# Kernel optimization log

Measured on AMD Instinct MI355X. Metric: run time of the kernel, lower is better.

## Reference

```python
import jax, jax.numpy as jnp
import numpy as np

RES = 16; NC = 256; NCP = 1024; KNN = 32; SIGMA = 0.1
DM = 256; NH = 8; FF = 1024; NLAYERS = 2
E = NC * 8 * (RES // 8) ** 2
EH = 8
B = 4; N = 65536


def setup_inputs() -> dict:
    key = jax.random.key(0)
    ks = jax.random.split(key, 16)
    s = 0.02
    def w(k, shape):
        return jax.random.normal(k, shape, jnp.float32) * s
    inp = {}
    inp['pc'] = jax.random.normal(ks[0], (B, N, 3), jnp.float32)
    inp['pe_w1'] = w(ks[1], (3, 128)); inp['pe_b1'] = jnp.zeros((128,), jnp.float32)
    inp['pe_w2'] = w(ks[2], (128, 128)); inp['pe_b2'] = jnp.zeros((128,), jnp.float32)
    inp['t_qkv_w'] = w(ks[3], (NLAYERS, DM, 3 * DM)); inp['t_qkv_b'] = jnp.zeros((NLAYERS, 3 * DM), jnp.float32)
    inp['t_out_w'] = w(ks[4], (NLAYERS, DM, DM)); inp['t_out_b'] = jnp.zeros((NLAYERS, DM), jnp.float32)
    inp['t_ln1_s'] = jnp.ones((NLAYERS, DM), jnp.float32); inp['t_ln1_b'] = jnp.zeros((NLAYERS, DM), jnp.float32)
    inp['t_ff1_w'] = w(ks[5], (NLAYERS, DM, FF)); inp['t_ff1_b'] = jnp.zeros((NLAYERS, FF), jnp.float32)
    inp['t_ff2_w'] = w(ks[6], (NLAYERS, FF, DM)); inp['t_ff2_b'] = jnp.zeros((NLAYERS, DM), jnp.float32)
    inp['t_ln2_s'] = jnp.ones((NLAYERS, DM), jnp.float32); inp['t_ln2_b'] = jnp.zeros((NLAYERS, DM), jnp.float32)
    inp['c1_w'] = w(ks[7], (2 * NC, NC, 3, 3)); inp['c1_b'] = jnp.zeros((2 * NC,), jnp.float32)
    inp['c2_w'] = w(ks[8], (4 * NC, 2 * NC, 3, 3)); inp['c2_b'] = jnp.zeros((4 * NC,), jnp.float32)
    inp['c3_w'] = w(ks[9], (8 * NC, 4 * NC, 3, 3)); inp['c3_b'] = jnp.zeros((8 * NC,), jnp.float32)
    inp['x_qkv_w'] = w(ks[10], (E, 3 * E)); inp['x_qkv_b'] = jnp.zeros((3 * E,), jnp.float32)
    inp['x_out_w'] = w(ks[11], (E, E)); inp['x_out_b'] = jnp.zeros((E,), jnp.float32)
    return inp


def _layernorm(x, s, b):
    m = x.mean(-1, keepdims=True)
    v = ((x - m) ** 2).mean(-1, keepdims=True)
    return (x - m) / jnp.sqrt(v + 1e-5) * s + b


def _mha(x, qkv_w, qkv_b, out_w, out_b, nh):
    Bq, S, D = x.shape
    dh = D // nh
    qkv = x @ qkv_w + qkv_b
    q, k, v = jnp.split(qkv, 3, axis=-1)
    def sp(t):
        return t.reshape(Bq, S, nh, dh).transpose(0, 2, 1, 3)
    q, k, v = sp(q), sp(k), sp(v)
    a = jax.nn.softmax(jnp.einsum('bhqd,bhkd->bhqk', q, k) / jnp.sqrt(jnp.float32(dh)), axis=-1)
    o = jnp.einsum('bhqk,bhkd->bhqd', a, v).transpose(0, 2, 1, 3).reshape(Bq, S, D)
    return o @ out_w + out_b


def _density(pc):
    # faithful to source: distance to the FIRST k points (unsorted), not kNN
    d = jnp.linalg.norm(pc[:, :, None, :] - pc[:, None, :KNN, :], axis=-1)  # (B,N,k)
    return jnp.exp(-2.0 * SIGMA ** 2 / (d * d + 1e-6)).mean(axis=-1)


def _fps_indices(pc, density):
    # incremental min-dist FPS: selects identical points to the original O(N*K^2) loop
    def one(pc_b, dens_b):
        first = jnp.argmax(dens_b)
        mind = jnp.linalg.norm(pc_b - pc_b[first], axis=-1)
        def step(mind, _):
            idx = jnp.argmax(mind)
            d = jnp.linalg.norm(pc_b - pc_b[idx], axis=-1)
            return jnp.minimum(mind, d), idx
        _, rest = jax.lax.scan(step, mind, None, length=NCP - 1)
        return jnp.concatenate([first[None], rest])
    return jax.vmap(one)(pc, density)


def _forward(pc, idx, pe_w1, pe_b1, pe_w2, pe_b2, t_qkv_w, t_qkv_b, t_out_w, t_out_b,
             t_ln1_s, t_ln1_b, t_ff1_w, t_ff1_b, t_ff2_w, t_ff2_b, t_ln2_s, t_ln2_b,
             c1_w, c1_b, c2_w, c2_b, c3_w, c3_b, x_qkv_w, x_qkv_b, x_out_w, x_out_b):
    Bq = pc.shape[0]
    centers = jnp.take_along_axis(pc, idx[:, :, None], axis=1)  # (B,K,3)
    # point encoder MLP -> (B,K,128)
    f = jax.nn.relu(centers @ pe_w1 + pe_b1) @ pe_w2 + pe_b2
    # sinusoidal pos-emb per axis, mean over xyz -> (B,K,128)
    half = 64
    freqs = jnp.exp(jnp.arange(half, dtype=jnp.float32) * (-np.log(10000.0) / (half - 1)))
    e = centers[..., None] * freqs  # (B,K,3,64)
    pos = jnp.concatenate([jnp.sin(e), jnp.cos(e)], axis=-1).mean(axis=2)
    x = jnp.concatenate([f, pos], axis=-1)  # (B,K,256)
    # 2-layer post-LN transformer encoder
    for l in range(NLAYERS):
        h = _mha(x, t_qkv_w[l], t_qkv_b[l], t_out_w[l], t_out_b[l], NH)
        x = _layernorm(x + h, t_ln1_s[l], t_ln1_b[l])
        h = jax.nn.relu(x @ t_ff1_w[l] + t_ff1_b[l]) @ t_ff2_w[l] + t_ff2_b[l]
        x = _layernorm(x + h, t_ln2_s[l], t_ln2_b[l])
    # scatter-add features onto three planes
    L = pc.max() - pc.min()
    def grid(c):
        return jnp.clip(((c + L / 2) / L * RES).astype(jnp.int32), 0, RES - 1)
    gx = grid(centers[..., 0]); gy = grid(centers[..., 1]); gz = grid(centers[..., 2])
    tri = jnp.zeros((Bq, 3, RES, RES, DM), jnp.float32)  # channels last for scatter
    bi = jnp.arange(Bq)[:, None]
    tri = tri.at[bi, 0, gy, gx].add(x)
    tri = tri.at[bi, 1, gz, gy].add(x)
    tri = tri.at[bi, 2, gz, gx].add(x)
    tri = tri.transpose(0, 1, 4, 2, 3)  # (B,3,C,R,R)
    z = tri.reshape(Bq * 3, DM, RES, RES)
    def conv(xx, w, b):
        y = jax.lax.conv_general_dilated(xx, w, (2, 2), ((1, 1), (1, 1)),
                                         dimension_numbers=('NCHW', 'OIHW', 'NCHW'))
        return y + b[None, :, None, None]
    z = jax.nn.relu(conv(z, c1_w, c1_b))
    z = jax.nn.relu(conv(z, c2_w, c2_b))
    z = jax.nn.relu(conv(z, c3_w, c3_b))  # (B*3, 8C, R/8, R/8)
    flat = z.reshape(Bq, 3, E)
    attn = _mha(flat, x_qkv_w, x_qkv_b, x_out_w, x_out_b, EH)
    return attn.reshape(Bq, 3, 8 * NC, RES // 8, RES // 8)


def reference(pc, pe_w1, pe_b1, pe_w2, pe_b2, t_qkv_w, t_qkv_b, t_out_w, t_out_b,
              t_ln1_s, t_ln1_b, t_ff1_w, t_ff1_b, t_ff2_w, t_ff2_b, t_ln2_s, t_ln2_b,
              c1_w, c1_b, c2_w, c2_b, c3_w, c3_b, x_qkv_w, x_qkv_b, x_out_w, x_out_b):
    idx = _fps_indices(pc, _density(pc))
    return _forward(pc, idx, pe_w1, pe_b1, pe_w2, pe_b2, t_qkv_w, t_qkv_b, t_out_w, t_out_b,
                    t_ln1_s, t_ln1_b, t_ff1_w, t_ff1_b, t_ff2_w, t_ff2_b, t_ln2_s, t_ln2_b,
                    c1_w, c1_b, c2_w, c2_b, c3_w, c3_b, x_qkv_w, x_qkv_b, x_out_w, x_out_b)
```

## Files before the change

### kernel.cpp

```cpp
#include <hip/hip_runtime.h>
#include <math.h>

#define NPTS   65536
#define NBATCH 4
#define KCP    1024
#define DM     256
#define FFD    1024
#define EDIM   8192
#define N3E    24576

#define FPS_NBLK 16
#define FPS_THR  256
#define FPS_PPT  16
#define GPUB     8
#define HARV_MAX 16
#define RING     16

__device__ __forceinline__ unsigned long long umaxll(unsigned long long a, unsigned long long b) {
  return a > b ? a : b;
}

__global__ __launch_bounds__(256) void redmm_kernel(const float* __restrict__ v, int n,
                                                    float* __restrict__ pmax, float* __restrict__ pmin) {
  float mx = -INFINITY, mn = INFINITY;
  for (int i = blockIdx.x * 256 + threadIdx.x; i < n; i += gridDim.x * 256) {
    float x = v[i]; mx = fmaxf(mx, x); mn = fminf(mn, x);
  }
#pragma unroll
  for (int off = 32; off >= 1; off >>= 1) {
    mx = fmaxf(mx, __shfl_xor(mx, off, 64));
    mn = fminf(mn, __shfl_xor(mn, off, 64));
  }
  __shared__ float smx[4], smn[4];
  int lane = threadIdx.x & 63, w = threadIdx.x >> 6;
  if (lane == 0) { smx[w] = mx; smn[w] = mn; }
  __syncthreads();
  if (threadIdx.x == 0) {
    pmax[blockIdx.x] = fmaxf(fmaxf(smx[0], smx[1]), fmaxf(smx[2], smx[3]));
    pmin[blockIdx.x] = fminf(fminf(smn[0], smn[1]), fminf(smn[2], smn[3]));
  }
}

__global__ __launch_bounds__(256) void redfin_kernel(const float* __restrict__ pmax,
                                                     const float* __restrict__ pmin, int nb,
                                                     float* __restrict__ Lv) {
  float mx = -INFINITY, mn = INFINITY;
  for (int i = threadIdx.x; i < nb; i += 256) { mx = fmaxf(mx, pmax[i]); mn = fminf(mn, pmin[i]); }
#pragma unroll
  for (int off = 32; off >= 1; off >>= 1) {
    mx = fmaxf(mx, __shfl_xor(mx, off, 64));
    mn = fminf(mn, __shfl_xor(mn, off, 64));
  }
  __shared__ float smx[4], smn[4];
  int lane = threadIdx.x & 63, w = threadIdx.x >> 6;
  if (lane == 0) { smx[w] = mx; smn[w] = mn; }
  __syncthreads();
  if (threadIdx.x == 0) {
    mx = fmaxf(fmaxf(smx[0], smx[1]), fmaxf(smx[2], smx[3]));
    mn = fminf(fminf(smn[0], smn[1]), fminf(smn[2], smn[3]));
    Lv[0] = __fsub_rn(mx, mn);
  }
}

__global__ __launch_bounds__(FPS_THR, 1) void fps_kernel(const float* __restrict__ pc,
                                                         float* __restrict__ centers,
                                                         unsigned* __restrict__ tags,
                                                         unsigned long long* __restrict__ keys) {
  const int blk = blockIdx.x;
  const int b = blk / FPS_NBLK, bb = blk % FPS_NBLK;
  const int tid = threadIdx.x;
  const int lane = tid & 63, wv = tid >> 6;
  const int wvg = bb * 4 + wv;
  const float* pcb = pc + (size_t)b * NPTS * 3;

  __shared__ float kpts[96];

  float px[FPS_PPT], py[FPS_PPT], pz[FPS_PPT], mind[FPS_PPT];
  const int gbase = wvg * 1024;
#pragma unroll
  for (int i = 0; i < FPS_PPT; ++i) {
    int g = gbase + i * 64 + lane;
    px[i] = pcb[3 * g]; py[i] = pcb[3 * g + 1]; pz[i] = pcb[3 * g + 2];
  }
  for (int i = tid; i < 96; i += FPS_THR) kpts[i] = pcb[i];
  __syncthreads();

  unsigned* const tagb = tags + (size_t)b * RING * 64;
  unsigned long long* const keyb = keys + (size_t)b * RING * 512;

  auto exchange = [&](const unsigned long long* ek, int nk, int r,
                      unsigned long long* ck) {
    const int ri = r & (RING - 1);
    if (lane == 0) {
      unsigned long long* sp = keyb + (size_t)ri * 512 + wvg * 8;
      for (int g = 0; g < nk; ++g)
        __hip_atomic_store(&sp[g], ek[g], __ATOMIC_RELAXED, __HIP_MEMORY_SCOPE_AGENT);
      __hip_atomic_store(&tagb[ri * 64 + wvg], (unsigned)r, __ATOMIC_RELEASE, __HIP_MEMORY_SCOPE_AGENT);
    }
    unsigned tag;
    do {
      tag = __hip_atomic_load(&tagb[ri * 64 + lane], __ATOMIC_ACQUIRE, __HIP_MEMORY_SCOPE_AGENT);
    } while (__any(tag != (unsigned)r));
    const unsigned long long* pl = keyb + (size_t)ri * 512 + lane * 8;
    for (int e = 0; e < nk; ++e)
      ck[e] = __hip_atomic_load(&pl[e], __ATOMIC_RELAXED, __HIP_MEMORY_SCOPE_AGENT);
  };

  {
    unsigned long long bk = 0ull;
#pragma unroll
    for (int i = 0; i < FPS_PPT; ++i) {
      float acc = 0.f;
      for (int j = 0; j < 32; ++j) {
        float dx = __fsub_rn(px[i], kpts[3 * j]);
        float dy = __fsub_rn(py[i], kpts[3 * j + 1]);
        float dz = __fsub_rn(pz[i], kpts[3 * j + 2]);
        float ss = __fadd_rn(__fadd_rn(__fmul_rn(dx, dx), __fmul_rn(dy, dy)), __fmul_rn(dz, dz));
        float d = __fsqrt_rn(ss);
        float dd = __fadd_rn(__fmul_rn(d, d), 1e-6f);
        acc = __fadd_rn(acc, expf(__fdiv_rn(-0.02f, dd)));
      }
      float dens = __fdiv_rn(acc, 32.f);
      int g = gbase + i * 64 + lane;
      bk = umaxll(bk, ((unsigned long long)__float_as_uint(dens) << 32) | (unsigned int)(~g));
    }
#pragma unroll
    for (int off = 1; off < 64; off <<= 1) bk = umaxll(bk, __shfl_xor(bk, off, 64));
    unsigned long long ek[1] = { bk }, ck[1];
    exchange(ek, 1, 1, ck);
    unsigned long long k2 = ck[0];
#pragma unroll
    for (int off = 1; off < 64; off <<= 1) k2 = umaxll(k2, __shfl_xor(k2, off, 64));
    int widx = (int)(~(unsigned)(k2 & 0xFFFFFFFFull));
    float wx = pcb[3 * widx], wy = pcb[3 * widx + 1], wz = pcb[3 * widx + 2];
    if (wvg == 0 && lane == 0) {
      centers[(size_t)b * KCP * 3 + 0] = wx;
      centers[(size_t)b * KCP * 3 + 1] = wy;
      centers[(size_t)b * KCP * 3 + 2] = wz;
    }
#pragma unroll
    for (int i = 0; i < FPS_PPT; ++i) {
      float dx = __fsub_rn(px[i], wx), dy = __fsub_rn(py[i], wy), dz = __fsub_rn(pz[i], wz);
      mind[i] = __fsqrt_rn(__fadd_rn(__fadd_rn(__fmul_rn(dx, dx), __fmul_rn(dy, dy)), __fmul_rn(dz, dz)));
    }
  }

  int t = 1;
  for (int r = 2; t < KCP; ++r) {
    unsigned long long tk[FPS_PPT];
#pragma unroll
    for (int i = 0; i < FPS_PPT; ++i) {
      int g = gbase + i * 64 + lane;
      tk[i] = ((unsigned long long)__float_as_uint(mind[i]) << 32) | (unsigned int)(~g);
    }
    unsigned long long ek[GPUB];
#pragma unroll
    for (int g = 0; g < GPUB; ++g) {
      unsigned long long lbk = 0ull;
#pragma unroll
      for (int i = 0; i < FPS_PPT; ++i) lbk = umaxll(lbk, tk[i]);
      unsigned long long wk = lbk;
#pragma unroll
      for (int off = 1; off < 64; off <<= 1) wk = umaxll(wk, __shfl_xor(wk, off, 64));
      ek[g] = wk;
#pragma unroll
      for (int i = 0; i < FPS_PPT; ++i)
        if (tk[i] == wk) tk[i] = 0ull;
    }
    unsigned long long ck[GPUB];
    exchange(ek, GPUB, r, ck);
    float cx[GPUB], cy[GPUB], cz[GPUB];
#pragma unroll
    for (int e = 0; e < GPUB; ++e) {
      int gi = (int)(~(unsigned)(ck[e] & 0xFFFFFFFFull));
      cx[e] = pcb[3 * gi]; cy[e] = pcb[3 * gi + 1]; cz[e] = pcb[3 * gi + 2];
    }
    unsigned long long u = ck[GPUB - 1];
#pragma unroll
    for (int off = 1; off < 64; off <<= 1) u = umaxll(u, __shfl_xor(u, off, 64));
    int h = 0;
    while (true) {
      unsigned long long lb = 0ull; float lx = 0.f, ly = 0.f, lz = 0.f;
#pragma unroll
      for (int e = 0; e < GPUB; ++e)
        if (ck[e] > lb) { lb = ck[e]; lx = cx[e]; ly = cy[e]; lz = cz[e]; }
      unsigned long long wk = lb;
#pragma unroll
      for (int off = 1; off < 64; off <<= 1) wk = umaxll(wk, __shfl_xor(wk, off, 64));
      if (h > 0 && wk < u) break;
      int owner = __ffsll(__ballot(lb == wk)) - 1;
      float wx = __shfl(lx, owner, 64), wy = __shfl(ly, owner, 64), wz = __shfl(lz, owner, 64);
      if (wvg == 0 && lane == 0) {
        centers[((size_t)b * KCP + t) * 3 + 0] = wx;
        centers[((size_t)b * KCP + t) * 3 + 1] = wy;
        centers[((size_t)b * KCP + t) * 3 + 2] = wz;
      }
#pragma unroll
      for (int e = 0; e < GPUB; ++e) {
        float dx = __fsub_rn(cx[e], wx), dy = __fsub_rn(cy[e], wy), dz = __fsub_rn(cz[e], wz);
        float d = __fsqrt_rn(__fadd_rn(__fadd_rn(__fmul_rn(dx, dx), __fmul_rn(dy, dy)), __fmul_rn(dz, dz)));
        float ov = __uint_as_float((unsigned)(ck[e] >> 32));
        float nv = fminf(ov, d);
        ck[e] = ((unsigned long long)__float_as_uint(nv) << 32) | (ck[e] & 0xFFFFFFFFull);
      }
#pragma unroll
      for (int i = 0; i < FPS_PPT; ++i) {
        float dx = __fsub_rn(px[i], wx), dy = __fsub_rn(py[i], wy), dz = __fsub_rn(pz[i], wz);
        float d = __fsqrt_rn(__fadd_rn(__fadd_rn(__fmul_rn(dx, dx), __fmul_rn(dy, dy)), __fmul_rn(dz, dz)));
        mind[i] = fminf(mind[i], d);
      }
      ++h; ++t;
      if (h == HARV_MAX || t == KCP) break;
    }
  }
}

__global__ __launch_bounds__(128) void pe_kernel(const float* __restrict__ centers,
                                                 const float* __restrict__ w1, const float* __restrict__ b1,
                                                 const float* __restrict__ w2, const float* __restrict__ b2,
                                                 float* __restrict__ x) {
  const int p = blockIdx.x;
  const int d = threadIdx.x;
  __shared__ float h[128];
  __shared__ float c[3];
  if (d < 3) c[d] = centers[(size_t)p * 3 + d];
  __syncthreads();
  float hv = b1[d];
#pragma unroll
  for (int j = 0; j < 3; ++j) hv += c[j] * w1[j * 128 + d];
  hv = fmaxf(hv, 0.f);
  h[d] = hv;
  __syncthreads();
  float f = b2[d];
  for (int j = 0; j < 128; ++j) f += h[j] * w2[j * 128 + d];
  x[(size_t)p * 256 + d] = f;
  if (d < 64) {
    float fr = expf(__fmul_rn((float)d, -0.14619587892025696f));
    float ssum = 0.f, csum = 0.f;
#pragma unroll
    for (int a = 0; a < 3; ++a) {
      float e = __fmul_rn(c[a], fr);
      ssum += sinf(e); csum += cosf(e);
    }
    x[(size_t)p * 256 + 128 + d] = __fdiv_rn(ssum, 3.f);
    x[(size_t)p * 256 + 192 + d] = __fdiv_rn(csum, 3.f);
  }
}

__global__ __launch_bounds__(256) void gemm_kernel(const float* __restrict__ A, const float* __restrict__ W,
                                                   const float* __restrict__ bias, float* __restrict__ C,
                                                   int M, int Kd, int Nd, int relu) {
  __shared__ float As[16][65];
  __shared__ float Ws[16][65];
  const int bm = blockIdx.y * 64, bn = blockIdx.x * 64;
  const int tid = threadIdx.x;
  const int tx = tid & 15, ty = tid >> 4;
  float acc[4][4] = {};
  for (int k0 = 0; k0 < Kd; k0 += 16) {
#pragma unroll
    for (int i = 0; i < 4; ++i) {
      int f = tid + 256 * i; int k = f & 15, m = f >> 4;
      As[k][m] = A[(size_t)(bm + m) * Kd + k0 + k];
    }
#pragma unroll
    for (int i = 0; i < 4; ++i) {
      int f = tid + 256 * i; int n = f & 63, k = f >> 6;
      Ws[k][n] = W[(size_t)(k0 + k) * Nd + bn + n];
    }
    __syncthreads();
#pragma unroll
    for (int k = 0; k < 16; ++k) {
      float a[4], w[4];
#pragma unroll
      for (int i = 0; i < 4; ++i) a[i] = As[k][ty * 4 + i];
#pragma unroll
      for (int j = 0; j < 4; ++j) w[j] = Ws[k][tx * 4 + j];
#pragma unroll
      for (int i = 0; i < 4; ++i)
#pragma unroll
        for (int j = 0; j < 4; ++j) acc[i][j] += a[i] * w[j];
    }
    __syncthreads();
  }
#pragma unroll
  for (int i = 0; i < 4; ++i)
#pragma unroll
    for (int j = 0; j < 4; ++j) {
      float v = acc[i][j] + bias[bn + tx * 4 + j];
      if (relu) v = fmaxf(v, 0.f);
      C[(size_t)(bm + ty * 4 + i) * Nd + bn + tx * 4 + j] = v;
    }
}

__global__ __launch_bounds__(256, 1) void flash_kernel(const float* __restrict__ qkv, float* __restrict__ ao) {
  const int qt = blockIdx.x, h = blockIdx.y, b = blockIdx.z;
  const int tid = threadIdx.x;
  const int qi = tid >> 2, p = tid & 3;
  const int q0 = qt * 64;
  __shared__ float Kc[64][36];
  __shared__ float Vc[64][36];
  __shared__ float Sc[64][68];

  float4 q4[8];
  const float* qrow = qkv + (size_t)(b * 1024 + q0 + qi) * 768 + h * 32;
#pragma unroll
  for (int i = 0; i < 8; ++i) q4[i] = ((const float4*)qrow)[i];

  float o0[4] = {0, 0, 0, 0}, o1[4] = {0, 0, 0, 0};
  float m_cur = -INFINITY, l_part = 0.f;
  const int d0 = p * 8;

  for (int c0 = 0; c0 < 1024; c0 += 64) {
    for (int i = tid; i < 64 * 32; i += 256) {
      int j = i >> 5, d = i & 31;
      size_t row = (size_t)(b * 1024 + c0 + j) * 768;
      Kc[j][d] = qkv[row + 256 + h * 32 + d];
      Vc[j][d] = qkv[row + 512 + h * 32 + d];
    }
    __syncthreads();
    float sreg[16];
#pragma unroll 4
    for (int jj = 0; jj < 16; ++jj) {
      int j = p + 4 * jj;
      const float* kr = &Kc[j][0];
      float s = 0.f;
#pragma unroll
      for (int i = 0; i < 8; ++i) {
        float4 kv = *(const float4*)(kr + 4 * i);
        s += q4[i].x * kv.x + q4[i].y * kv.y + q4[i].z * kv.z + q4[i].w * kv.w;
      }
      sreg[jj] = s * 0.17677669529663687f;
    }
    float cmax = sreg[0];
#pragma unroll
    for (int jj = 1; jj < 16; ++jj) cmax = fmaxf(cmax, sreg[jj]);
    cmax = fmaxf(cmax, __shfl_xor(cmax, 1, 64));
    cmax = fmaxf(cmax, __shfl_xor(cmax, 2, 64));
    float m_new = fmaxf(m_cur, cmax);
    float corr = expf(m_cur - m_new);
    l_part *= corr;
#pragma unroll
    for (int i = 0; i < 4; ++i) { o0[i] *= corr; o1[i] *= corr; }
#pragma unroll
    for (int jj = 0; jj < 16; ++jj) {
      float pv = expf(sreg[jj] - m_new);
      l_part += pv;
      Sc[qi][p + 4 * jj] = pv;
    }
    m_cur = m_new;
    for (int j = 0; j < 64; ++j) {
      float pj = Sc[qi][j];
      float4 va = *(const float4*)(&Vc[j][d0]);
      float4 vb = *(const float4*)(&Vc[j][d0 + 4]);
      o0[0] += pj * va.x; o0[1] += pj * va.y; o0[2] += pj * va.z; o0[3] += pj * va.w;
      o1[0] += pj * vb.x; o1[1] += pj * vb.y; o1[2] += pj * vb.z; o1[3] += pj * vb.w;
    }
    __syncthreads();
  }
  float l2 = l_part + __shfl_xor(l_part, 1, 64);
  float lt = l2 + __shfl_xor(l2, 2, 64);
  float inv = 1.f / lt;
  float* orow = ao + (size_t)(b * 1024 + q0 + qi) * 256 + h * 32 + d0;
#pragma unroll
  for (int i = 0; i < 4; ++i) orow[i] = o0[i] * inv;
#pragma unroll
  for (int i = 0; i < 4; ++i) orow[4 + i] = o1[i] * inv;
}

__global__ __launch_bounds__(256) void ln_kernel(const float* __restrict__ a, const float* __restrict__ r,
                                                 const float* __restrict__ sc, const float* __restrict__ bi,
                                                 float* __restrict__ out) {
  const int row = blockIdx.x * 4 + (threadIdx.x >> 6);
  const int lane = threadIdx.x & 63;
  const float* ar = a + (size_t)row * 256;
  const float* rr = r + (size_t)row * 256;
  float v[4];
#pragma unroll
  for (int i = 0; i < 4; ++i) v[i] = ar[lane + 64 * i] + rr[lane + 64 * i];
  float s = v[0] + v[1] + v[2] + v[3];
#pragma unroll
  for (int off = 32; off >= 1; off >>= 1) s += __shfl_xor(s, off, 64);
  float mean = s * (1.f / 256.f);
  float vs = 0.f;
#pragma unroll
  for (int i = 0; i < 4; ++i) { float d = v[i] - mean; vs += d * d; }
#pragma unroll
  for (int off = 32; off >= 1; off >>= 1) vs += __shfl_xor(vs, off, 64);
  float var = vs * (1.f / 256.f);
  float rstd = 1.f / sqrtf(var + 1e-5f);
  float* orow = out + (size_t)row * 256;
#pragma unroll
  for (int i = 0; i < 4; ++i) {
    int d = lane + 64 * i;
    orow[d] = (v[i] - mean) * rstd * sc[d] + bi[d];
  }
}

__global__ __launch_bounds__(256) void scatter_kernel(const float* __restrict__ x,
                                                      const float* __restrict__ centers,
                                                      const float* __restrict__ Lv,
                                                      float* __restrict__ tri) {
  const int pnt = blockIdx.x;
  const int b = pnt >> 10;
  const int tid = threadIdx.x;
  __shared__ int g[3];
  if (tid == 0) {
    float L = Lv[0];
    float half = __fmul_rn(L, 0.5f);
#pragma unroll
    for (int a = 0; a < 3; ++a) {
      float c = centers[(size_t)pnt * 3 + a];
      float t = __fmul_rn(__fdiv_rn(__fadd_rn(c, half), L), 16.f);
      int gi = (int)t;
      g[a] = min(15, max(0, gi));
    }
  }
  __syncthreads();
  const int gx = g[0], gy = g[1], gz = g[2];
  float v = x[(size_t)pnt * 256 + tid];
  float* trib = tri + (size_t)b * 3 * 256 * 256;
  atomicAdd(&trib[(0 * 256 + tid) * 256 + gy * 16 + gx], v);
  atomicAdd(&trib[(1 * 256 + tid) * 256 + gz * 16 + gy], v);
  atomicAdd(&trib[(2 * 256 + tid) * 256 + gz * 16 + gx], v);
}

template <int IC, int OC, int IH, int IW, int OH, int OW, int OCT, int ICC>
__global__ __launch_bounds__(256, 1) void conv_kernel(const float* __restrict__ in, const float* __restrict__ w,
                                                      const float* __restrict__ bias, float* __restrict__ out) {
  __shared__ float lin[ICC * IH * IW];
  const int n = blockIdx.x;
  const int oc = blockIdx.y * OCT + threadIdx.x / (OH * OW);
  const int sp = threadIdx.x % (OH * OW);
  const int oy = sp / OW, ox = sp % OW;
  const int iy0 = oy * 2 - 1, ix0 = ox * 2 - 1;
  float acc = 0.f;
  for (int c0 = 0; c0 < IC; c0 += ICC) {
    __syncthreads();
    for (int i = threadIdx.x; i < ICC * IH * IW; i += 256)
      lin[i] = in[((size_t)n * IC + c0) * (IH * IW) + i];
    __syncthreads();
    const float* wp = w + ((size_t)oc * IC + c0) * 9;
    for (int ic = 0; ic < ICC; ++ic) {
      const float* wr = wp + (size_t)ic * 9;
      const float* lr = lin + ic * IH * IW;
#pragma unroll
      for (int ky = 0; ky < 3; ++ky) {
        int iy = iy0 + ky;
        if (iy >= 0 && iy < IH) {
#pragma unroll
          for (int kx = 0; kx < 3; ++kx) {
            int ix = ix0 + kx;
            if (ix >= 0 && ix < IW) acc += lr[iy * IW + ix] * wr[ky * 3 + kx];
          }
        }
      }
    }
  }
  out[((size_t)n * OC + oc) * (OH * OW) + sp] = fmaxf(acc + bias[oc], 0.f);
}

__global__ void biasinit_kernel(float* __restrict__ out, const float* __restrict__ bias, int M, int N) {
  int i = blockIdx.x * 256 + threadIdx.x;
  if (i < M * N) out[i] = bias[i % N];
}

template <int M, int KC>
__global__ __launch_bounds__(256, 1) void matvec_kernel(const float* __restrict__ A, const float* __restrict__ W,
                                                        float* __restrict__ out, int Kd, int Nd) {
  __shared__ float Al[KC * M];
  const int tid = threadIdx.x;
  const int n = blockIdx.x * 256 + tid;
  const int k0 = blockIdx.y * KC;
  for (int i = tid; i < KC * M; i += 256) {
    int k = i / M, m = i - k * M;
    Al[i] = A[(size_t)m * Kd + k0 + k];
  }
  __syncthreads();
  float acc[M] = {};
  for (int k = 0; k < KC; ++k) {
    float wv = W[(size_t)(k0 + k) * Nd + n];
#pragma unroll
    for (int m = 0; m < M; ++m) acc[m] += Al[k * M + m] * wv;
  }
#pragma unroll
  for (int m = 0; m < M; ++m) atomicAdd(&out[(size_t)m * Nd + n], acc[m]);
}

__global__ __launch_bounds__(256) void attn3_kernel(const float* __restrict__ qkv, float* __restrict__ o) {
  const int b = blockIdx.x >> 3, h = blockIdx.x & 7;
  const float* base = qkv + (size_t)b * 3 * N3E;
  const int qo = h * 1024, ko = EDIM + h * 1024, vo = 2 * EDIM + h * 1024;
  float p[9] = {};
  for (int d = threadIdx.x; d < 1024; d += 256) {
    float q0 = base[qo + d], q1 = base[N3E + qo + d], q2 = base[2 * N3E + qo + d];
    float k0 = base[ko + d], k1 = base[N3E + ko + d], k2 = base[2 * N3E + ko + d];
    p[0] += q0 * k0; p[1] += q0 * k1; p[2] += q0 * k2;
    p[3] += q1 * k0; p[4] += q1 * k1; p[5] += q1 * k2;
    p[6] += q2 * k0; p[7] += q2 * k1; p[8] += q2 * k2;
  }
  __shared__ float red[4][9];
  __shared__ float aw[9];
  const int lane = threadIdx.x & 63, w = threadIdx.x >> 6;
#pragma unroll
  for (int e = 0; e < 9; ++e)
#pragma unroll
    for (int off = 32; off >= 1; off >>= 1) p[e] += __shfl_xor(p[e], off, 64);
  if (lane == 0)
#pragma unroll
    for (int e = 0; e < 9; ++e) red[w][e] = p[e];
  __syncthreads();
  if (threadIdx.x == 0) {
    float s[9];
#pragma unroll
    for (int e = 0; e < 9; ++e) s[e] = (red[0][e] + red[1][e] + red[2][e] + red[3][e]) / 32.f;
#pragma unroll
    for (int i = 0; i < 3; ++i) {
      float m = fmaxf(fmaxf(s[i * 3], s[i * 3 + 1]), s[i * 3 + 2]);
      float e0 = expf(s[i * 3] - m), e1 = expf(s[i * 3 + 1] - m), e2 = expf(s[i * 3 + 2] - m);
      float sm = e0 + e1 + e2;
      aw[i * 3] = e0 / sm; aw[i * 3 + 1] = e1 / sm; aw[i * 3 + 2] = e2 / sm;
    }
  }
  __syncthreads();
  for (int d = threadIdx.x; d < 1024; d += 256) {
    float v0 = base[vo + d], v1 = base[N3E + vo + d], v2 = base[2 * N3E + vo + d];
#pragma unroll
    for (int i = 0; i < 3; ++i)
      o[(size_t)(b * 3 + i) * EDIM + h * 1024 + d] = aw[i * 3] * v0 + aw[i * 3 + 1] * v1 + aw[i * 3 + 2] * v2;
  }
}

extern "C" void kernel_launch(void* const* d_in, const int* in_sizes, int n_in,
                              void* d_out, int out_size, void* d_ws, size_t ws_size,
                              hipStream_t stream) {
  const float* pc      = (const float*)d_in[0];
  const float* pe_w1   = (const float*)d_in[1];
  const float* pe_b1   = (const float*)d_in[2];
  const float* pe_w2   = (const float*)d_in[3];
  const float* pe_b2   = (const float*)d_in[4];
  const float* t_qkv_w = (const float*)d_in[5];
  const float* t_qkv_b = (const float*)d_in[6];
  const float* t_out_w = (const float*)d_in[7];
  const float* t_out_b = (const float*)d_in[8];
  const float* t_ln1_s = (const float*)d_in[9];
  const float* t_ln1_b = (const float*)d_in[10];
  const float* t_ff1_w = (const float*)d_in[11];
  const float* t_ff1_b = (const float*)d_in[12];
  const float* t_ff2_w = (const float*)d_in[13];
  const float* t_ff2_b = (const float*)d_in[14];
  const float* t_ln2_s = (const float*)d_in[15];
  const float* t_ln2_b = (const float*)d_in[16];
  const float* c1_w    = (const float*)d_in[17];
  const float* c1_b    = (const float*)d_in[18];
  const float* c2_w    = (const float*)d_in[19];
  const float* c2_b    = (const float*)d_in[20];
  const float* c3_w    = (const float*)d_in[21];
  const float* c3_b    = (const float*)d_in[22];
  const float* x_qkv_w = (const float*)d_in[23];
  const float* x_qkv_b = (const float*)d_in[24];
  const float* x_out_w = (const float*)d_in[25];
  const float* x_out_b = (const float*)d_in[26];
  float* outp = (float*)d_out;

  char* wsp = (char*)d_ws;
  auto alloc = [&](size_t bytes) { char* q = wsp; wsp += (bytes + 255) & ~(size_t)255; return q; };
  float* centers = (float*)alloc((size_t)NBATCH * KCP * 3 * 4);
  float* pmax    = (float*)alloc(512 * 4);
  float* pmin    = (float*)alloc(512 * 4);
  float* Lv      = (float*)alloc(256);
  unsigned* tags = (unsigned*)alloc((size_t)NBATCH * RING * 64 * 4);
  unsigned long long* keyss = (unsigned long long*)alloc((size_t)NBATCH * RING * 512 * 8);
  float* x  = (float*)alloc((size_t)4096 * 256 * 4);
  float* xb = (float*)alloc((size_t)4096 * 256 * 4);
  float* arena = (float*)wsp;
  float* qkvb = arena;
  float* ao   = qkvb + (size_t)4096 * 768;
  float* po   = ao + (size_t)4096 * 256;
  float* ffh  = po + (size_t)4096 * 256;
  float* ffo  = ffh + (size_t)4096 * 1024;
  float* tri  = arena;
  float* z1   = tri + (size_t)NBATCH * 3 * 256 * 256;
  float* z2   = z1 + (size_t)12 * 512 * 64;
  float* z3   = z2 + (size_t)12 * 1024 * 16;
  float* qkv2 = z3 + (size_t)12 * 8192;
  float* at2  = qkv2 + (size_t)12 * N3E;
  (void)in_sizes; (void)n_in; (void)out_size; (void)ws_size; (void)ffo;

  hipMemsetAsync(tags, 0, (size_t)NBATCH * RING * 64 * 4 + 256 + (size_t)NBATCH * RING * 512 * 8, stream);

  redmm_kernel<<<512, 256, 0, stream>>>(pc, NBATCH * NPTS * 3, pmax, pmin);
  redfin_kernel<<<1, 256, 0, stream>>>(pmax, pmin, 512, Lv);

  fps_kernel<<<NBATCH * FPS_NBLK, FPS_THR, 0, stream>>>(pc, centers, tags, keyss);

  pe_kernel<<<NBATCH * KCP, 128, 0, stream>>>(centers, pe_w1, pe_b1, pe_w2, pe_b2, x);

  for (int l = 0; l < 2; ++l) {
    gemm_kernel<<<dim3(12, 64), 256, 0, stream>>>(x, t_qkv_w + (size_t)l * 256 * 768,
                                                  t_qkv_b + (size_t)l * 768, qkvb, 4096, 256, 768, 0);
    flash_kernel<<<dim3(16, 8, 4), 256, 0, stream>>>(qkvb, ao);
    gemm_kernel<<<dim3(4, 64), 256, 0, stream>>>(ao, t_out_w + (size_t)l * 256 * 256,
                                                 t_out_b + (size_t)l * 256, po, 4096, 256, 256, 0);
    ln_kernel<<<1024, 256, 0, stream>>>(x, po, t_ln1_s + (size_t)l * 256, t_ln1_b + (size_t)l * 256, xb);
    gemm_kernel<<<dim3(16, 64), 256, 0, stream>>>(xb, t_ff1_w + (size_t)l * 256 * 1024,
                                                  t_ff1_b + (size_t)l * 1024, ffh, 4096, 256, 1024, 1);
    gemm_kernel<<<dim3(4, 64), 256, 0, stream>>>(ffh, t_ff2_w + (size_t)l * 1024 * 256,
                                                 t_ff2_b + (size_t)l * 256, ffo, 4096, 1024, 256, 0);
    ln_kernel<<<1024, 256, 0, stream>>>(xb, ffo, t_ln2_s + (size_t)l * 256, t_ln2_b + (size_t)l * 256, x);
  }

  hipMemsetAsync(tri, 0, (size_t)NBATCH * 3 * 256 * 256 * 4, stream);
  scatter_kernel<<<NBATCH * KCP, 256, 0, stream>>>(x, centers, Lv, tri);

  conv_kernel<256, 512, 16, 16, 8, 8, 4, 32><<<dim3(12, 128), 256, 0, stream>>>(tri, c1_w, c1_b, z1);
  conv_kernel<512, 1024, 8, 8, 4, 4, 16, 128><<<dim3(12, 64), 256, 0, stream>>>(z1, c2_w, c2_b, z2);
  conv_kernel<1024, 2048, 4, 4, 2, 2, 64, 256><<<dim3(12, 32), 256, 0, stream>>>(z2, c3_w, c3_b, z3);

  biasinit_kernel<<<(12 * N3E + 255) / 256, 256, 0, stream>>>(qkv2, x_qkv_b, 12, N3E);
  matvec_kernel<12, 512><<<dim3(N3E / 256, 16), 256, 0, stream>>>(z3, x_qkv_w, qkv2, EDIM, N3E);

  attn3_kernel<<<32, 256, 0, stream>>>(qkv2, at2);

  biasinit_kernel<<<(12 * EDIM + 255) / 256, 256, 0, stream>>>(outp, x_out_b, 12, EDIM);
  matvec_kernel<12, 512><<<dim3(EDIM / 256, 16), 256, 0, stream>>>(at2, x_out_w, outp, EDIM, EDIM);
}
```

Measured before the change: 5.320 ms.

## Replace scalar FP32 transformer GEMMs with bf16 MFMA tiled kernel

Swaps the scalar 64x64-tile FP32 GEMM used for the transformer QKV, output, and FFN projections for a 128x128-tile kernel. The new kernel converts A and W to bf16 while staging them in shared memory and uses 16x16x32 bf16 MFMA instructions, with each of four waves computing a 64x64 sub-tile. This is meant to cut GEMM compute time by using the matrix cores. In exchange it lowers input precision to bf16, launches fewer blocks, and loads W with strided scalar reads.

```diff
diff --git a/kernel.cpp b/kernel.cpp
--- a/kernel.cpp
+++ b/kernel.cpp
@@ -16,8 +16,17 @@
 #define HARV_MAX 16
 #define RING     16
 
+typedef __attribute__((ext_vector_type(8))) short short8v;
+typedef __attribute__((ext_vector_type(4))) short short4v;
+typedef __attribute__((ext_vector_type(4))) float float4v;
+
 __device__ __forceinline__ unsigned long long umaxll(unsigned long long a, unsigned long long b) {
   return a > b ? a : b;
+}
+
+__device__ __forceinline__ short bf16rn(float f) {
+  unsigned u = __float_as_uint(f);
+  return (short)((u + 0x7FFFu + ((u >> 16) & 1u)) >> 16);
 }
 
 __global__ __launch_bounds__(256) void redmm_kernel(const float* __restrict__ v, int n,
@@ -247,49 +256,75 @@
   }
 }
 
-__global__ __launch_bounds__(256) void gemm_kernel(const float* __restrict__ A, const float* __restrict__ W,
-                                                   const float* __restrict__ bias, float* __restrict__ C,
-                                                   int M, int Kd, int Nd, int relu) {
-  __shared__ float As[16][65];
-  __shared__ float Ws[16][65];
-  const int bm = blockIdx.y * 64, bn = blockIdx.x * 64;
+__global__ __launch_bounds__(256) void gemm_mfma_kernel(const float* __restrict__ A,
+                                                        const float* __restrict__ W,
+                                                        const float* __restrict__ bias,
+                                                        float* __restrict__ C,
+                                                        int M, int Kd, int Nd, int relu) {
+  __shared__ short Al[128][40];
+  __shared__ short Wl[128][40];
+  const int bm = blockIdx.y * 128, bn = blockIdx.x * 128;
   const int tid = threadIdx.x;
-  const int tx = tid & 15, ty = tid >> 4;
-  float acc[4][4] = {};
-  for (int k0 = 0; k0 < Kd; k0 += 16) {
+  const int lane = tid & 63, wv = tid >> 6;
+  const int wr = wv >> 1, wc = wv & 1;
+  const int l15 = lane & 15, lk = lane >> 4;
+
+  float4v acc[4][4];
+#pragma unroll
+  for (int i = 0; i < 4; ++i)
+#pragma unroll
+    for (int j = 0; j < 4; ++j) acc[i][j] = (float4v){0.f, 0.f, 0.f, 0.f};
+
+  for (int k0 = 0; k0 < Kd; k0 += 32) {
+    __syncthreads();
 #pragma unroll
     for (int i = 0; i < 4; ++i) {
-      int f = tid + 256 * i; int k = f & 15, m = f >> 4;
-      As[k][m] = A[(size_t)(bm + m) * Kd + k0 + k];
+      int idx = (i * 256 + tid) * 4;
+      int m = idx >> 5, k = idx & 31;
+      float4 v = *(const float4*)&A[(size_t)(bm + m) * Kd + k0 + k];
+      short4v s = { bf16rn(v.x), bf16rn(v.y), bf16rn(v.z), bf16rn(v.w) };
+      *(short4v*)&Al[m][k] = s;
     }
 #pragma unroll
     for (int i = 0; i < 4; ++i) {
-      int f = tid + 256 * i; int n = f & 63, k = f >> 6;
-      Ws[k][n] = W[(size_t)(k0 + k) * Nd + bn + n];
+      int task = i * 256 + tid;
+      int n = task & 127, c = task >> 7;
+      short4v s;
+#pragma unroll
+      for (int j = 0; j < 4; ++j)
+        s[j] = bf16rn(W[(size_t)(k0 + c * 4 + j) * Nd + bn + n]);
+      *(short4v*)&Wl[n][c * 4] = s;
     }
     __syncthreads();
-#pragma unroll
-    for (int k = 0; k < 16; ++k) {
-      float a[4], w[4];
-#pragma unroll
-      for (int i = 0; i < 4; ++i) a[i] = As[k][ty * 4 + i];
-#pragma unroll
-      for (int j = 0; j < 4; ++j) w[j] = Ws[k][tx * 4 + j];
-#pragma unroll
-      for (int i = 0; i < 4; ++i)
-#pragma unroll
-        for (int j = 0; j < 4; ++j) acc[i][j] += a[i] * w[j];
-    }
-    __syncthreads();
-  }
-#pragma unroll
-  for (int i = 0; i < 4; ++i)
-#pragma unroll
-    for (int j = 0; j < 4; ++j) {
-      float v = acc[i][j] + bias[bn + tx * 4 + j];
-      if (relu) v = fmaxf(v, 0.f);
-      C[(size_t)(bm + ty * 4 + i) * Nd + bn + tx * 4 + j] = v;
-    }
+    short8v af[4], bf[4];
+#pragma unroll
+    for (int mf = 0; mf < 4; ++mf)
+      af[mf] = *(const short8v*)&Al[wr * 64 + mf * 16 + l15][lk * 8];
+#pragma unroll
+    for (int nf = 0; nf < 4; ++nf)
+      bf[nf] = *(const short8v*)&Wl[wc * 64 + nf * 16 + l15][lk * 8];
+#pragma unroll
+    for (int mf = 0; mf < 4; ++mf)
+#pragma unroll
+      for (int nf = 0; nf < 4; ++nf)
+        acc[mf][nf] = __builtin_amdgcn_mfma_f32_16x16x32_bf16(af[mf], bf[nf], acc[mf][nf], 0, 0, 0);
+  }
+
+#pragma unroll
+  for (int mf = 0; mf < 4; ++mf) {
+    int row = bm + wr * 64 + mf * 16 + lk * 4;
+#pragma unroll
+    for (int nf = 0; nf < 4; ++nf) {
+      int col = bn + wc * 64 + nf * 16 + l15;
+      float bv = bias[col];
+#pragma unroll
+      for (int j = 0; j < 4; ++j) {
+        float v = acc[mf][nf][j] + bv;
+        if (relu) v = fmaxf(v, 0.f);
+        C[(size_t)(row + j) * Nd + col] = v;
+      }
+    }
+  }
 }
 
 __global__ __launch_bounds__(256, 1) void flash_kernel(const float* __restrict__ qkv, float* __restrict__ ao) {
@@ -596,16 +631,16 @@
   pe_kernel<<<NBATCH * KCP, 128, 0, stream>>>(centers, pe_w1, pe_b1, pe_w2, pe_b2, x);
 
   for (int l = 0; l < 2; ++l) {
-    gemm_kernel<<<dim3(12, 64), 256, 0, stream>>>(x, t_qkv_w + (size_t)l * 256 * 768,
-                                                  t_qkv_b + (size_t)l * 768, qkvb, 4096, 256, 768, 0);
+    gemm_mfma_kernel<<<dim3(6, 32), 256, 0, stream>>>(x, t_qkv_w + (size_t)l * 256 * 768,
+                                                      t_qkv_b + (size_t)l * 768, qkvb, 4096, 256, 768, 0);
     flash_kernel<<<dim3(16, 8, 4), 256, 0, stream>>>(qkvb, ao);
-    gemm_kernel<<<dim3(4, 64), 256, 0, stream>>>(ao, t_out_w + (size_t)l * 256 * 256,
-                                                 t_out_b + (size_t)l * 256, po, 4096, 256, 256, 0);
+    gemm_mfma_kernel<<<dim3(2, 32), 256, 0, stream>>>(ao, t_out_w + (size_t)l * 256 * 256,
+                                                      t_out_b + (size_t)l * 256, po, 4096, 256, 256, 0);
     ln_kernel<<<1024, 256, 0, stream>>>(x, po, t_ln1_s + (size_t)l * 256, t_ln1_b + (size_t)l * 256, xb);
-    gemm_kernel<<<dim3(16, 64), 256, 0, stream>>>(xb, t_ff1_w + (size_t)l * 256 * 1024,
-                                                  t_ff1_b + (size_t)l * 1024, ffh, 4096, 256, 1024, 1);
-    gemm_kernel<<<dim3(4, 64), 256, 0, stream>>>(ffh, t_ff2_w + (size_t)l * 1024 * 256,
-                                                 t_ff2_b + (size_t)l * 256, ffo, 4096, 1024, 256, 0);
+    gemm_mfma_kernel<<<dim3(8, 32), 256, 0, stream>>>(xb, t_ff1_w + (size_t)l * 256 * 1024,
+                                                      t_ff1_b + (size_t)l * 1024, ffh, 4096, 256, 1024, 1);
+    gemm_mfma_kernel<<<dim3(2, 32), 256, 0, stream>>>(ffh, t_ff2_w + (size_t)l * 1024 * 256,
+                                                      t_ff2_b + (size_t)l * 256, ffo, 4096, 1024, 256, 0);
     ln_kernel<<<1024, 256, 0, stream>>>(xb, ffo, t_ln2_s + (size_t)l * 256, t_ln2_b + (size_t)l * 256, x);
   }
 
```

Result: faster. 5.016 ms (-5.7%).
